# Performance work log

Hardware: AMD Instinct MI355X
Metric: run time of the kernel (lower is better)

## Reference

```python
import jax, jax.numpy as jnp
import numpy as np

B, T, NIN, H1, H2, E, A = 256, 128, 1024, 512, 512, 256, 16
EPS = 1e-5


def setup_inputs() -> dict:
    key = jax.random.key(0)
    ks = jax.random.split(key, 24)
    def lin(k, fan_in, fan_out):
        # weights stored [in, out]; y = x @ W + b (equivalent to torch Linear)
        s = 1.0 / np.sqrt(fan_in)
        kw, kb = jax.random.split(k)
        return (jax.random.uniform(kw, (fan_in, fan_out), jnp.float32, -s, s),
                jax.random.uniform(kb, (fan_out,), jnp.float32, -s, s))
    W1, b1 = lin(ks[0], NIN, H1)
    W2, b2 = lin(ks[1], H1, H2)
    W3, b3 = lin(ks[2], H2, E)
    Wih, bih = lin(ks[3], E, 3 * E)   # GRUCell input weights, gate order [r, z, n]
    Whh, bhh = lin(ks[4], E, 3 * E)   # GRUCell hidden weights
    Whe, bhe = lin(ks[5], E + A, E)   # hidden_encoder
    Wae, bae = lin(ks[6], A, A)       # action_encoder
    return {
        'obs': jax.random.normal(ks[7], (B, T, NIN), jnp.float32),
        'actions': jax.random.normal(ks[8], (B, T, A), jnp.float32),
        'W1': W1, 'b1': b1, 'g1': jnp.ones((H1,), jnp.float32), 'be1': jnp.zeros((H1,), jnp.float32),
        'W2': W2, 'b2': b2, 'g2': jnp.ones((H2,), jnp.float32), 'be2': jnp.zeros((H2,), jnp.float32),
        'W3': W3, 'b3': b3,
        'Wih': Wih, 'bih': bih, 'Whh': Whh, 'bhh': bhh,
        'Whe': Whe, 'bhe': bhe, 'Wae': Wae, 'bae': bae,
    }


def reference(obs, actions, W1, b1, g1, be1, W2, b2, g2, be2, W3, b3,
              Wih, bih, Whh, bhh, Whe, bhe, Wae, bae):
    def bn(x, g, b):  # BatchNorm1d, training mode (batch stats, biased var)
        mu = jnp.mean(x, axis=0)
        var = jnp.mean((x - mu) ** 2, axis=0)
        return g * (x - mu) / jnp.sqrt(var + EPS) + b

    def mlp(x):
        x = jax.nn.elu(bn(x @ W1 + b1, g1, be1))
        x = jax.nn.elu(bn(x @ W2 + b2, g2, be2))
        return x @ W3 + b3

    def gru(x, h):
        gi = x @ Wih + bih
        gh = h @ Whh + bhh
        ir, iz, inn = jnp.split(gi, 3, axis=1)
        hr, hz, hn = jnp.split(gh, 3, axis=1)
        r = jax.nn.sigmoid(ir + hr)
        z = jax.nn.sigmoid(iz + hz)
        n = jnp.tanh(inn + r * hn)
        return (1.0 - z) * n + z * h

    obs_t = jnp.swapaxes(obs, 0, 1)       # [T, B, NIN]
    act_t = jnp.swapaxes(actions, 0, 1)   # [T, B, A]
    h0 = jnp.zeros((obs.shape[0], E), jnp.float32)
    a0 = jnp.zeros((obs.shape[0], A), jnp.float32)

    def step(carry, xs):
        h, a_prev = carry
        o, a = xs
        h = jnp.concatenate([h, a_prev], axis=1) @ Whe + bhe
        a_prev = a @ Wae + bae
        h = gru(mlp(o), h)
        return (h, a_prev), None

    (h, _), _ = jax.lax.scan(step, (h0, a0), (obs_t, act_t))
    return h
```

## Files before the change

kernel.cpp:

```cpp
#include <hip/hip_runtime.h>
#include <math.h>
#include <stdint.h>

#define B_   256
#define T_   128
#define NIN_ 1024
#define H1_  512
#define E_   256
#define A_   16
#define MT_  (B_ * T_)

typedef unsigned short ushort_t;
typedef __attribute__((ext_vector_type(8))) short   short8;
typedef __attribute__((ext_vector_type(8))) __bf16  bf16x8;
typedef __attribute__((ext_vector_type(4))) float   f32x4;

union frag8 { short8 s; bf16x8 b; };

__device__ __forceinline__ ushort_t f2bf(float f) {
  union { float f; unsigned u; } v; v.f = f;
  unsigned r = (v.u + 0x7FFFu + ((v.u >> 16) & 1u)) >> 16;
  return (ushort_t)r;
}

static constexpr size_t OFF_C0    = 0;
static constexpr size_t OFF_OBSB  = 0;
static constexpr size_t OFF_Y     = 134217728;
static constexpr size_t OFF_YG    = 134217728;
static constexpr size_t OFF_XG    = 167772160;
static constexpr size_t OFF_PENCB = 184549376;
static constexpr size_t OFF_XB    = 201326592;
static constexpr size_t OFF_INN   = 201326592;
static constexpr size_t OFF_AE    = 234881024;
static constexpr size_t OFF_W1T   = 236978176;
static constexpr size_t OFF_W2T   = 238026752;
static constexpr size_t OFF_W3T   = 238551040;
static constexpr size_t OFF_WIHT  = 239075328;
static constexpr size_t OFF_WHHT  = 239468544;
static constexpr size_t OFF_WCT   = 240123904;
static constexpr size_t OFF_BSUM  = 241172480;
static constexpr size_t OFF_FLAGS = 241176576;
static constexpr size_t OFF_HG    = 241238016;


__global__ __launch_bounds__(256) void cast_obs_k(const float* __restrict__ obs,
                                                  ushort_t* __restrict__ out) {
  int row_in = blockIdx.x;
  int b = row_in / T_, t = row_in - b * T_;
  const float4* s4 = (const float4*)(obs + (size_t)row_in * NIN_);
  float4 v = s4[threadIdx.x];
  ushort_t* d = out + (size_t)(t * B_ + b) * NIN_ + threadIdx.x * 4;
  d[0] = f2bf(v.x); d[1] = f2bf(v.y); d[2] = f2bf(v.z); d[3] = f2bf(v.w);
}

__global__ __launch_bounds__(256) void transpose_cast_k(const float* __restrict__ in,
                                                        ushort_t* __restrict__ out,
                                                        int R, int C) {
  __shared__ float tile[32][33];
  int c0 = blockIdx.x * 32, r0 = blockIdx.y * 32;
  int tx = threadIdx.x & 31, ty = threadIdx.x >> 5;
  for (int i = 0; i < 4; i++) {
    int r = r0 + ty * 4 + i;
    if (r < R && (c0 + tx) < C) tile[ty * 4 + i][tx] = in[(size_t)r * C + c0 + tx];
  }
  __syncthreads();
  for (int i = 0; i < 4; i++) {
    int c = c0 + ty * 4 + i, r = r0 + tx;
    if (c < C && r < R) out[(size_t)c * R + r] = f2bf(tile[tx][ty * 4 + i]);
  }
}

__global__ __launch_bounds__(256) void wct_a_k(const float* __restrict__ Whe,
                                               ushort_t* __restrict__ Wct) {
  int c = blockIdx.x, k = threadIdx.x;
  Wct[(size_t)c * 256 + k] = f2bf(Whe[(size_t)k * 256 + c]);
}

__global__ __launch_bounds__(256) void wct_b_k(const float* __restrict__ Whe,
                                               const float* __restrict__ Whh,
                                               ushort_t* __restrict__ Wct) {
  int c = blockIdx.x;
  int k = threadIdx.x;
  float acc = 0.f;
  for (int j = 0; j < 256; j++)
    acc += Whe[(size_t)k * 256 + j] * Whh[(size_t)j * 768 + c];
  Wct[(size_t)(256 + c) * 256 + k] = f2bf(acc);
}

__global__ void bsum_k(const float* __restrict__ bih, const float* __restrict__ bhh,
                       float* __restrict__ bs) {
  int i = blockIdx.x * 256 + threadIdx.x;
  if (i < 768) bs[i] = bih[i] + bhh[i];
}

__global__ void init_flags_k(unsigned* f) {
  if (threadIdx.x < 16) f[threadIdx.x * 32] = 0u;
}

__global__ __launch_bounds__(256) void ae_k(const float* __restrict__ actions,
                                            const float* __restrict__ Wae,
                                            const float* __restrict__ bae,
                                            float* __restrict__ AE) {
  int idx = blockIdx.x * 256 + threadIdx.x;
  int m = idx >> 4, k2 = idx & 15;
  int t = m >> 8, b = m & 255;
  const float* arow = actions + ((size_t)b * T_ + t) * A_;
  float acc = bae[k2];
  for (int k = 0; k < 16; k++) acc += arow[k] * Wae[k * 16 + k2];
  AE[(size_t)m * 16 + k2] = acc;
}

__global__ __launch_bounds__(256) void penc_k(const float* __restrict__ AE,
                                              const float* __restrict__ Whe,
                                              const float* __restrict__ bhe,
                                              float* __restrict__ C0,
                                              ushort_t* __restrict__ Pencb) {
  int m = blockIdx.x;
  int j = threadIdx.x;
  __shared__ float a[16];
  if (threadIdx.x < 16)
    a[threadIdx.x] = (m >= B_) ? AE[(size_t)(m - B_) * 16 + threadIdx.x] : 0.f;
  __syncthreads();
  float acc = bhe[j];
  if (m >= B_) {
    for (int k = 0; k < 16; k++) acc += a[k] * Whe[(size_t)(256 + k) * 256 + j];
  }
  C0[(size_t)m * 1024 + j] = acc;
  Pencb[(size_t)m * 256 + j] = f2bf(acc);
}

__global__ __launch_bounds__(512) void bn_elu_k(const float* __restrict__ Y,
                                                const float* __restrict__ g,
                                                const float* __restrict__ be,
                                                ushort_t* __restrict__ Xb) {
  int t = blockIdx.x, f = threadIdx.x;
  const float* base = Y + (size_t)t * B_ * H1_;
  float s = 0.f, ss = 0.f;
  for (int b = 0; b < B_; b++) {
    float v = base[(size_t)b * H1_ + f];
    s += v; ss += v * v;
  }
  float mu  = s * (1.f / B_);
  float var = ss * (1.f / B_) - mu * mu;
  float inv = 1.f / sqrtf(var + 1e-5f);
  float sc = g[f] * inv, sh = be[f] - mu * sc;
  ushort_t* ob = Xb + (size_t)t * B_ * H1_;
  for (int b = 0; b < B_; b++) {
    float v = base[(size_t)b * H1_ + f] * sc + sh;
    float e = v > 0.f ? v : (expf(v) - 1.f);
    ob[(size_t)b * H1_ + f] = f2bf(e);
  }
}

__global__ __launch_bounds__(256) void cast_k(const float* __restrict__ in,
                                              ushort_t* __restrict__ out, long n) {
  long i = (long)blockIdx.x * 256 + threadIdx.x;
  if (i < n) out[i] = f2bf(in[i]);
}

__global__ __launch_bounds__(256) void gemm_bt_k(const ushort_t* __restrict__ A, int lda,
                                                 const ushort_t* __restrict__ Bt, int ldb,
                                                 float* __restrict__ C, int ldc,
                                                 const float* __restrict__ bias,
                                                 int K, int accum) {
  __shared__ __align__(16) ushort_t As[128][40];
  __shared__ __align__(16) ushort_t Bs[128][40];
  int tid = threadIdx.x;
  int wave = tid >> 6, lane = tid & 63;
  int q = lane >> 4, l15 = lane & 15;
  int wr = wave >> 1, wc = wave & 1;
  int m0 = blockIdx.x * 128, n0 = blockIdx.y * 128;
  f32x4 acc[4][4] = {};
  int r = tid >> 1, sh = (tid & 1) * 16;
  const ushort_t* aSrc = A + (size_t)(m0 + r) * lda + sh;
  const ushort_t* bSrc = Bt + (size_t)(n0 + r) * ldb + sh;
  for (int k0 = 0; k0 < K; k0 += 32) {
    *(short8*)&As[r][sh]     = *(const short8*)(aSrc + k0);
    *(short8*)&As[r][sh + 8] = *(const short8*)(aSrc + k0 + 8);
    *(short8*)&Bs[r][sh]     = *(const short8*)(bSrc + k0);
    *(short8*)&Bs[r][sh + 8] = *(const short8*)(bSrc + k0 + 8);
    __syncthreads();
    frag8 af[4], bf[4];
#pragma unroll
    for (int i = 0; i < 4; i++) {
      af[i].s = *(const short8*)&As[wr * 64 + i * 16 + l15][q * 8];
      bf[i].s = *(const short8*)&Bs[wc * 64 + i * 16 + l15][q * 8];
    }
#pragma unroll
    for (int at = 0; at < 4; at++)
#pragma unroll
      for (int bt = 0; bt < 4; bt++)
        acc[at][bt] = __builtin_amdgcn_mfma_f32_16x16x32_bf16(af[at].b, bf[bt].b, acc[at][bt], 0, 0, 0);
    __syncthreads();
  }
#pragma unroll
  for (int at = 0; at < 4; at++)
#pragma unroll
    for (int bt = 0; bt < 4; bt++) {
      int mb = m0 + wr * 64 + at * 16 + q * 4;
      int n  = n0 + wc * 64 + bt * 16 + l15;
      float bv = bias ? bias[n] : 0.f;
#pragma unroll
      for (int i = 0; i < 4; i++) {
        size_t idx = (size_t)(mb + i) * ldc + n;
        float v = acc[at][bt][i] + bv;
        if (accum) v += C[idx];
        C[idx] = v;
      }
    }
}

__global__ __launch_bounds__(1024) void gru_cols_k(
    const ushort_t* __restrict__ Wct,
    const float* __restrict__ C0,
    const float* __restrict__ INN,
    unsigned* __restrict__ hG,
    unsigned* __restrict__ flags,
    float* __restrict__ outF) {
  __shared__ __align__(16) ushort_t Wb[256][264];
  __shared__ __align__(16) ushort_t h_lds[16][264];
  __shared__ float G[4][16][66];

  const int tid = threadIdx.x;
  const int w = tid >> 6, lane = tid & 63;
  const int q = lane >> 4, l15 = lane & 15;
  const int rg = blockIdx.x & 15, cg = blockIdx.x >> 4;
  const int r0 = rg * 16;
  const int g = w >> 2, j = w & 3;

  unsigned* flag = flags + rg * 32;

  for (int d = tid; d < 16 * 264 / 2; d += 1024) ((unsigned*)h_lds)[d] = 0u;
  for (int i = tid; i < 256 * 32; i += 1024) {
    int rr = i >> 5, ss = i & 31;
    int srow = (rr >> 6) * 256 + cg * 64 + (rr & 63);
    *(short8*)&Wb[rr][ss * 8] = *(const short8*)(Wct + (size_t)srow * 256 + ss * 8);
  }
  __syncthreads();

  const int crow = tid >> 6;
  const int ccol = tid & 63;
  const int hg = cg * 64 + ccol;

  for (int t = 0; t < T_; t++) {
    const float* c0t  = C0  + ((size_t)t * B_ + r0) * 1024;
    const float* innt = INN + ((size_t)t * B_ + r0) * 256;
    float c0he = c0t[(size_t)crow * 1024 + hg];
    float c0r  = c0t[(size_t)crow * 1024 + 256 + hg];
    float c0z  = c0t[(size_t)crow * 1024 + 512 + hg];
    float c0hn = c0t[(size_t)crow * 1024 + 768 + hg];
    float c0in = innt[(size_t)crow * 256 + hg];

    if (t > 0) {
      if (tid == 0) {
        unsigned target = 4u * (unsigned)t;
        while (__hip_atomic_load(flag, __ATOMIC_ACQUIRE, __HIP_MEMORY_SCOPE_AGENT) < target)
          __builtin_amdgcn_s_sleep(1);
      }
      __syncthreads();
      const unsigned* hsrc = hG + (size_t)(t & 1) * 256 * 128;
      for (int d = tid; d < 1536; d += 1024) {
        int s = d >> 9;
        int cgs = s + (s >= cg ? 1 : 0);
        int row = (d >> 5) & 15, cp = d & 31;
        unsigned v = __hip_atomic_load(&hsrc[(size_t)(r0 + row) * 128 + cgs * 32 + cp],
                                       __ATOMIC_RELAXED, __HIP_MEMORY_SCOPE_AGENT);
        *(unsigned*)&h_lds[row][cgs * 64 + cp * 2] = v;
      }
      __syncthreads();
    }

    f32x4 acc = {};
#pragma unroll
    for (int kc = 0; kc < 8; kc++) {
      frag8 a, b;
      a.s = *(const short8*)&h_lds[l15][kc * 32 + q * 8];
      b.s = *(const short8*)&Wb[g * 64 + j * 16 + l15][kc * 32 + q * 8];
      acc = __builtin_amdgcn_mfma_f32_16x16x32_bf16(a.b, b.b, acc, 0, 0, 0);
    }
#pragma unroll
    for (int i = 0; i < 4; i++) G[g][q * 4 + i][j * 16 + l15] = acc[i];
    __syncthreads();

    float henc = G[0][crow][ccol] + c0he;
    float rp   = G[1][crow][ccol] + c0r;
    float zp   = G[2][crow][ccol] + c0z;
    float hn   = G[3][crow][ccol] + c0hn;
    float rgate = 1.f / (1.f + expf(-rp));
    float zgate = 1.f / (1.f + expf(-zp));
    float ng = tanhf(c0in + rgate * hn);
    float hv = (1.f - zgate) * ng + zgate * henc;

    if (t < T_ - 1) {
      h_lds[crow][cg * 64 + ccol] = f2bf(hv);
      __syncthreads();
      if (tid < 512) {
        int row2 = tid >> 5, cp = tid & 31;
        unsigned v = *(const unsigned*)&h_lds[row2][cg * 64 + cp * 2];
        unsigned* hdst = hG + (size_t)((t + 1) & 1) * 256 * 128;
        __hip_atomic_store(&hdst[(size_t)(r0 + row2) * 128 + cg * 32 + cp], v,
                           __ATOMIC_RELAXED, __HIP_MEMORY_SCOPE_AGENT);
      }
      __syncthreads();
      if (tid == 0)
        __hip_atomic_fetch_add(flag, 1u, __ATOMIC_RELEASE, __HIP_MEMORY_SCOPE_AGENT);
    } else {
      outF[(size_t)(r0 + crow) * 256 + hg] = hv;
    }
  }
}

extern "C" void kernel_launch(void* const* d_in, const int* in_sizes, int n_in,
                              void* d_out, int out_size, void* d_ws, size_t ws_size,
                              hipStream_t stream) {
  const float* obs     = (const float*)d_in[0];
  const float* actions = (const float*)d_in[1];
  const float* W1  = (const float*)d_in[2];
  const float* b1  = (const float*)d_in[3];
  const float* g1  = (const float*)d_in[4];
  const float* be1 = (const float*)d_in[5];
  const float* W2  = (const float*)d_in[6];
  const float* b2  = (const float*)d_in[7];
  const float* g2  = (const float*)d_in[8];
  const float* be2 = (const float*)d_in[9];
  const float* W3  = (const float*)d_in[10];
  const float* b3  = (const float*)d_in[11];
  const float* Wih = (const float*)d_in[12];
  const float* bih = (const float*)d_in[13];
  const float* Whh = (const float*)d_in[14];
  const float* bhh = (const float*)d_in[15];
  const float* Whe = (const float*)d_in[16];
  const float* bhe = (const float*)d_in[17];
  const float* Wae = (const float*)d_in[18];
  const float* bae = (const float*)d_in[19];

  char* ws = (char*)d_ws;
  float*    C0    = (float*)(ws + OFF_C0);
  ushort_t* obsb  = (ushort_t*)(ws + OFF_OBSB);
  float*    Y     = (float*)(ws + OFF_Y);
  float*    Yg    = (float*)(ws + OFF_YG);
  ushort_t* XG    = (ushort_t*)(ws + OFF_XG);
  ushort_t* Pencb = (ushort_t*)(ws + OFF_PENCB);
  ushort_t* Xb    = (ushort_t*)(ws + OFF_XB);
  float*    INN   = (float*)(ws + OFF_INN);
  float*    AE    = (float*)(ws + OFF_AE);
  ushort_t* W1t   = (ushort_t*)(ws + OFF_W1T);
  ushort_t* W2t   = (ushort_t*)(ws + OFF_W2T);
  ushort_t* W3t   = (ushort_t*)(ws + OFF_W3T);
  ushort_t* Wiht  = (ushort_t*)(ws + OFF_WIHT);
  ushort_t* Whht  = (ushort_t*)(ws + OFF_WHHT);
  ushort_t* Wct   = (ushort_t*)(ws + OFF_WCT);
  float*    bsum  = (float*)(ws + OFF_BSUM);
  unsigned* flags = (unsigned*)(ws + OFF_FLAGS);
  unsigned* hG    = (unsigned*)(ws + OFF_HG);
  float*    outF  = (float*)d_out;

  cast_obs_k<<<MT_, 256, 0, stream>>>(obs, obsb);
  transpose_cast_k<<<dim3(16, 32), 256, 0, stream>>>(W1, W1t, 1024, 512);
  transpose_cast_k<<<dim3(16, 16), 256, 0, stream>>>(W2, W2t, 512, 512);
  transpose_cast_k<<<dim3(8, 16),  256, 0, stream>>>(W3, W3t, 512, 256);
  transpose_cast_k<<<dim3(24, 8),  256, 0, stream>>>(Wih, Wiht, 256, 768);
  transpose_cast_k<<<dim3(24, 8),  256, 0, stream>>>(Whh, Whht, 256, 768);
  wct_a_k<<<256, 256, 0, stream>>>(Whe, Wct);
  wct_b_k<<<768, 256, 0, stream>>>(Whe, Whh, Wct);
  bsum_k<<<3, 256, 0, stream>>>(bih, bhh, bsum);
  init_flags_k<<<1, 64, 0, stream>>>(flags);
  ae_k<<<MT_ * 16 / 256, 256, 0, stream>>>(actions, Wae, bae, AE);

  gemm_bt_k<<<dim3(256, 4), 256, 0, stream>>>(obsb, 1024, W1t, 1024, Y, 512, b1, 1024, 0);
  bn_elu_k<<<T_, 512, 0, stream>>>(Y, g1, be1, Xb);
  gemm_bt_k<<<dim3(256, 4), 256, 0, stream>>>(Xb, 512, W2t, 512, Y, 512, b2, 512, 0);
  bn_elu_k<<<T_, 512, 0, stream>>>(Y, g2, be2, Xb);
  gemm_bt_k<<<dim3(256, 2), 256, 0, stream>>>(Xb, 512, W3t, 512, Yg, 256, b3, 512, 0);
  cast_k<<<MT_ * 256 / 256, 256, 0, stream>>>(Yg, XG, (long)MT_ * 256);

  penc_k<<<MT_, 256, 0, stream>>>(AE, Whe, bhe, C0, Pencb);
  gemm_bt_k<<<dim3(256, 4), 256, 0, stream>>>(XG, 256, Wiht, 256, C0 + 256, 1024, bsum, 256, 0);
  gemm_bt_k<<<dim3(256, 4), 256, 0, stream>>>(Pencb, 256, Whht, 256, C0 + 256, 1024, nullptr, 256, 1);
  gemm_bt_k<<<dim3(256, 2), 256, 0, stream>>>(Pencb, 256, Whht + 512 * 256, 256, C0 + 768, 1024, bhh + 512, 256, 0);
  gemm_bt_k<<<dim3(256, 2), 256, 0, stream>>>(XG, 256, Wiht + 512 * 256, 256, INN, 256, bih + 512, 256, 0);

  gru_cols_k<<<64, 1024, 0, stream>>>(Wct, C0, INN, hG, flags, outF);
}
```

Measured before the change: 1.202 ms.

## Cut GRU step barriers with LDS go-flag, 64-bit h exchange, per-wave publish

The recurrent GRU kernel replaces the block-wide barriers around the cross-block hidden-state exchange. One lane polls the global flag and releases the other waves through an LDS go variable. Each wave packs its bf16 outputs with shuffles and writes them straight to global memory as 64-bit stores, and an LDS counter lets the last wave bump the global flag. The aim is to shorten the serial per-timestep critical path, at the cost of subtler memory-ordering correctness. bn_elu is also split into two 256-thread blocks per timestep to double its block count.

```diff
diff --git a/kernel.cpp b/kernel.cpp
--- a/kernel.cpp
+++ b/kernel.cpp
@@ -11,6 +11,7 @@
 #define MT_  (B_ * T_)
 
 typedef unsigned short ushort_t;
+typedef unsigned long long ull_t;
 typedef __attribute__((ext_vector_type(8))) short   short8;
 typedef __attribute__((ext_vector_type(8))) __bf16  bf16x8;
 typedef __attribute__((ext_vector_type(4))) float   f32x4;
@@ -129,11 +130,11 @@
   Pencb[(size_t)m * 256 + j] = f2bf(acc);
 }
 
-__global__ __launch_bounds__(512) void bn_elu_k(const float* __restrict__ Y,
+__global__ __launch_bounds__(256) void bn_elu_k(const float* __restrict__ Y,
                                                 const float* __restrict__ g,
                                                 const float* __restrict__ be,
                                                 ushort_t* __restrict__ Xb) {
-  int t = blockIdx.x, f = threadIdx.x;
+  int t = blockIdx.x, f = blockIdx.y * 256 + threadIdx.x;
   const float* base = Y + (size_t)t * B_ * H1_;
   float s = 0.f, ss = 0.f;
   for (int b = 0; b < B_; b++) {
@@ -214,12 +215,13 @@
     const ushort_t* __restrict__ Wct,
     const float* __restrict__ C0,
     const float* __restrict__ INN,
-    unsigned* __restrict__ hG,
+    ull_t* __restrict__ hG,
     unsigned* __restrict__ flags,
     float* __restrict__ outF) {
   __shared__ __align__(16) ushort_t Wb[256][264];
   __shared__ __align__(16) ushort_t h_lds[16][264];
   __shared__ float G[4][16][66];
+  __shared__ unsigned go, lcnt;
 
   const int tid = threadIdx.x;
   const int w = tid >> 6, lane = tid & 63;
@@ -230,6 +232,7 @@
 
   unsigned* flag = flags + rg * 32;
 
+  if (tid == 0) { go = 0u; lcnt = 0u; }
   for (int d = tid; d < 16 * 264 / 2; d += 1024) ((unsigned*)h_lds)[d] = 0u;
   for (int i = tid; i < 256 * 32; i += 1024) {
     int rr = i >> 5, ss = i & 31;
@@ -238,8 +241,8 @@
   }
   __syncthreads();
 
-  const int crow = tid >> 6;
-  const int ccol = tid & 63;
+  const int crow = w;
+  const int ccol = lane;
   const int hg = cg * 64 + ccol;
 
   for (int t = 0; t < T_; t++) {
@@ -252,20 +255,26 @@
     float c0in = innt[(size_t)crow * 256 + hg];
 
     if (t > 0) {
-      if (tid == 0) {
-        unsigned target = 4u * (unsigned)t;
-        while (__hip_atomic_load(flag, __ATOMIC_ACQUIRE, __HIP_MEMORY_SCOPE_AGENT) < target)
-          __builtin_amdgcn_s_sleep(1);
-      }
-      __syncthreads();
-      const unsigned* hsrc = hG + (size_t)(t & 1) * 256 * 128;
-      for (int d = tid; d < 1536; d += 1024) {
-        int s = d >> 9;
+      if (w == 0) {
+        if (lane == 0) {
+          while (__hip_atomic_load(flag, __ATOMIC_ACQUIRE, __HIP_MEMORY_SCOPE_AGENT) < 4u * (unsigned)t)
+            __builtin_amdgcn_s_sleep(2);
+          __hip_atomic_store(&go, (unsigned)t, __ATOMIC_RELEASE, __HIP_MEMORY_SCOPE_WORKGROUP);
+        }
+      } else {
+        if (lane == 0) {
+          while (__hip_atomic_load(&go, __ATOMIC_ACQUIRE, __HIP_MEMORY_SCOPE_WORKGROUP) < (unsigned)t)
+            __builtin_amdgcn_s_sleep(1);
+        }
+      }
+      if (tid < 768) {
+        int s = tid >> 8;
         int cgs = s + (s >= cg ? 1 : 0);
-        int row = (d >> 5) & 15, cp = d & 31;
-        unsigned v = __hip_atomic_load(&hsrc[(size_t)(r0 + row) * 128 + cgs * 32 + cp],
-                                       __ATOMIC_RELAXED, __HIP_MEMORY_SCOPE_AGENT);
-        *(unsigned*)&h_lds[row][cgs * 64 + cp * 2] = v;
+        int rem = tid & 255;
+        int row = rem >> 4, cp = rem & 15;
+        ull_t v = __hip_atomic_load(&hG[(size_t)(t & 1) * 256 * 64 + (size_t)(r0 + row) * 64 + cgs * 16 + cp],
+                                    __ATOMIC_RELAXED, __HIP_MEMORY_SCOPE_AGENT);
+        *(ull_t*)&h_lds[row][cgs * 64 + cp * 4] = v;
       }
       __syncthreads();
     }
@@ -292,18 +301,22 @@
     float hv = (1.f - zgate) * ng + zgate * henc;
 
     if (t < T_ - 1) {
-      h_lds[crow][cg * 64 + ccol] = f2bf(hv);
-      __syncthreads();
-      if (tid < 512) {
-        int row2 = tid >> 5, cp = tid & 31;
-        unsigned v = *(const unsigned*)&h_lds[row2][cg * 64 + cp * 2];
-        unsigned* hdst = hG + (size_t)((t + 1) & 1) * 256 * 128;
-        __hip_atomic_store(&hdst[(size_t)(r0 + row2) * 128 + cg * 32 + cp], v,
-                           __ATOMIC_RELAXED, __HIP_MEMORY_SCOPE_AGENT);
-      }
-      __syncthreads();
-      if (tid == 0)
-        __hip_atomic_fetch_add(flag, 1u, __ATOMIC_RELEASE, __HIP_MEMORY_SCOPE_AGENT);
+      unsigned hvb = (unsigned)f2bf(hv);
+      h_lds[crow][cg * 64 + ccol] = (ushort_t)hvb;
+      unsigned p1 = (unsigned)__shfl_xor((int)hvb, 1);
+      unsigned v32 = hvb | (p1 << 16);
+      unsigned p2 = (unsigned)__shfl_xor((int)v32, 2);
+      if ((lane & 3) == 0) {
+        ull_t v64 = (ull_t)v32 | ((ull_t)p2 << 32);
+        __hip_atomic_store(&hG[(size_t)((t + 1) & 1) * 256 * 64 + (size_t)(r0 + crow) * 64 + cg * 16 + (lane >> 2)],
+                           v64, __ATOMIC_RELAXED, __HIP_MEMORY_SCOPE_AGENT);
+      }
+      asm volatile("s_waitcnt vmcnt(0)" ::: "memory");
+      if (lane == 0) {
+        unsigned old = __hip_atomic_fetch_add(&lcnt, 1u, __ATOMIC_ACQ_REL, __HIP_MEMORY_SCOPE_WORKGROUP);
+        if (old == 16u * (unsigned)t + 15u)
+          __hip_atomic_fetch_add(flag, 1u, __ATOMIC_RELEASE, __HIP_MEMORY_SCOPE_AGENT);
+      }
     } else {
       outF[(size_t)(r0 + crow) * 256 + hg] = hv;
     }
@@ -352,7 +365,7 @@
   ushort_t* Wct   = (ushort_t*)(ws + OFF_WCT);
   float*    bsum  = (float*)(ws + OFF_BSUM);
   unsigned* flags = (unsigned*)(ws + OFF_FLAGS);
-  unsigned* hG    = (unsigned*)(ws + OFF_HG);
+  ull_t*    hG    = (ull_t*)(ws + OFF_HG);
   float*    outF  = (float*)d_out;
 
   cast_obs_k<<<MT_, 256, 0, stream>>>(obs, obsb);
@@ -368,9 +381,9 @@
   ae_k<<<MT_ * 16 / 256, 256, 0, stream>>>(actions, Wae, bae, AE);
 
   gemm_bt_k<<<dim3(256, 4), 256, 0, stream>>>(obsb, 1024, W1t, 1024, Y, 512, b1, 1024, 0);
-  bn_elu_k<<<T_, 512, 0, stream>>>(Y, g1, be1, Xb);
+  bn_elu_k<<<dim3(T_, 2), 256, 0, stream>>>(Y, g1, be1, Xb);
   gemm_bt_k<<<dim3(256, 4), 256, 0, stream>>>(Xb, 512, W2t, 512, Y, 512, b2, 512, 0);
-  bn_elu_k<<<T_, 512, 0, stream>>>(Y, g2, be2, Xb);
+  bn_elu_k<<<dim3(T_, 2), 256, 0, stream>>>(Y, g2, be2, Xb);
   gemm_bt_k<<<dim3(256, 2), 256, 0, stream>>>(Xb, 512, W3t, 512, Yg, 256, b3, 512, 0);
   cast_k<<<MT_ * 256 / 256, 256, 0, stream>>>(Yg, XG, (long)MT_ * 256);
 
```

New measurement: 1.283 ms. 6.7% more time.
